# Kernel optimization log

Measured on AMD Instinct MI355X. Metric: run time of the kernel, lower is better.

The kernel has to match this reference:

```python
import jax, jax.numpy as jnp
import numpy as np

N_NODES = 100000
N_EDGES = 1600000
IN_CH, HID_CH, OUT_CH = 8, 64, 2


def setup_inputs() -> dict:
    key = jax.random.key(0)
    ks = jax.random.split(key, 8)
    x = jax.random.normal(ks[0], (N_NODES, IN_CH), dtype=jnp.float32)
    edge_index = jax.random.randint(ks[1], (2, N_EDGES), 0, N_NODES, dtype=jnp.int64)
    s1 = 1.0 / np.sqrt(IN_CH)
    s2 = 1.0 / np.sqrt(HID_CH)
    W_l1 = jax.random.normal(ks[2], (HID_CH, IN_CH), dtype=jnp.float32) * s1
    b_l1 = jax.random.normal(ks[3], (HID_CH,), dtype=jnp.float32) * s1
    W_r1 = jax.random.normal(ks[4], (HID_CH, IN_CH), dtype=jnp.float32) * s1
    W_l2 = jax.random.normal(ks[5], (OUT_CH, HID_CH), dtype=jnp.float32) * s2
    b_l2 = jax.random.normal(ks[6], (OUT_CH,), dtype=jnp.float32) * s2
    W_r2 = jax.random.normal(ks[7], (OUT_CH, HID_CH), dtype=jnp.float32) * s2
    return {"x": x, "edge_index": edge_index, "W_l1": W_l1, "b_l1": b_l1,
            "W_r1": W_r1, "W_l2": W_l2, "b_l2": b_l2, "W_r2": W_r2}


def _sage_conv(x, edge_index, W_l, b_l, W_r):
    # PyG SAGEConv (aggr='mean', root_weight=True):
    #   out = lin_l(mean_{j in N(i)} x_j) + lin_r(x_i)
    src, dst = edge_index[0], edge_index[1]
    n = x.shape[0]
    msgs = x[src]                                             # [E, F] gather
    summed = jax.ops.segment_sum(msgs, dst, num_segments=n)   # [N, F] scatter-add
    cnt = jax.ops.segment_sum(jnp.ones((src.shape[0],), x.dtype), dst,
                              num_segments=n)                 # [N]
    aggr = summed / jnp.maximum(cnt, 1.0)[:, None]            # scatter-mean
    return aggr @ W_l.T + b_l + x @ W_r.T


def reference(x, edge_index, W_l1, b_l1, W_r1, W_l2, b_l2, W_r2):
    h = _sage_conv(x, edge_index, W_l1, b_l1, W_r1)
    h = jax.nn.relu(h)
    # Dropout(0.3) is identity in eval mode (deterministic baseline).
    out = _sage_conv(h, edge_index, W_l2, b_l2, W_r2)
    return out
```

## Files before the change

kernel.cpp:

```cpp
#include <hip/hip_runtime.h>

#define N_NODES 100000
#define N_EDGES 1600000
#define IN_CH 8
#define HID_CH 64
#define OUT_CH 2

#define R2   512
#define RN   196
#define CAP  3584
#define BB   256
#define BCHUNK (N_EDGES / BB)

#define WS_CURSOR 0
#define WS_BUCKET 512
#define WS_OFFDEG (512 + R2 * CAP)
#define WS_G      (WS_OFFDEG + R2 * RN)

__global__ __launch_bounds__(512) void bucket_kernel(
        const int* __restrict__ src, const int* __restrict__ dst,
        int* __restrict__ cursor, int* __restrict__ bucket) {
    __shared__ int cnt[R2];
    __shared__ int base[R2];
    __shared__ int cur[R2];
    for (int i = threadIdx.x; i < R2; i += 512) { cnt[i] = 0; cur[i] = 0; }
    __syncthreads();
    const int* dch = dst + (size_t)blockIdx.x * BCHUNK;
    const int* sch = src + (size_t)blockIdx.x * BCHUNK;
    for (int j = threadIdx.x; j < BCHUNK; j += 512)
        atomicAdd(&cnt[(unsigned)dch[j] / RN], 1);
    __syncthreads();
    if (threadIdx.x < R2) {
        int c = cnt[threadIdx.x];
        base[threadIdx.x] = (c > 0) ? atomicAdd(&cursor[threadIdx.x], c) : 0;
    }
    __syncthreads();
    for (int j = threadIdx.x; j < BCHUNK; j += 512) {
        unsigned d = (unsigned)dch[j];
        unsigned r = d / RN;
        unsigned dl = d - r * RN;
        int slot = base[r] + atomicAdd(&cur[r], 1);
        if (slot < CAP)
            bucket[(size_t)r * CAP + slot] = (int)((dl << 17) | (unsigned)sch[j]);
    }
}

__global__ __launch_bounds__(256) void sage1_range(
        const int* __restrict__ bucket_g, const int* __restrict__ cursor,
        const float* __restrict__ x,
        const float* __restrict__ W_l1, const float* __restrict__ b_l1,
        const float* __restrict__ W_r1,
        const float* __restrict__ W_l2, const float* __restrict__ b_l2,
        const float* __restrict__ W_r2,
        int* __restrict__ bucket_w, int* __restrict__ offdeg,
        float* __restrict__ g, float* __restrict__ out_rt) {
    __shared__ int raw[CAP];
    __shared__ int seg[CAP];
    __shared__ int cnt[RN];
    __shared__ int cur[RN];
    __shared__ int sscan[256];
    __shared__ float sWl[HID_CH * IN_CH];
    __shared__ float sWr[HID_CH * IN_CH];
    __shared__ float sb[HID_CH];
    __shared__ float sWl2[OUT_CH * HID_CH];
    __shared__ float sWr2[OUT_CH * HID_CH];
    __shared__ float sb2[OUT_CH];

    int tid = threadIdx.x;
    for (int i = tid; i < HID_CH * IN_CH; i += 256) {
        sWl[i] = W_l1[i];
        sWr[i] = W_r1[i];
    }
    for (int i = tid; i < HID_CH; i += 256) sb[i] = b_l1[i];
    for (int i = tid; i < OUT_CH * HID_CH; i += 256) {
        sWl2[i] = W_l2[i];
        sWr2[i] = W_r2[i];
    }
    if (tid < OUT_CH) sb2[tid] = b_l2[tid];

    int r = blockIdx.x;
    int len = cursor[r];
    if (len > CAP) len = CAP;
    const int* bin = bucket_g + (size_t)r * CAP;
    for (int j = tid; j < len; j += 256) raw[j] = bin[j];
    if (tid < RN) cnt[tid] = 0;
    __syncthreads();

    for (int j = tid; j < len; j += 256) atomicAdd(&cnt[raw[j] >> 17], 1);
    __syncthreads();

    int v = (tid < RN) ? cnt[tid] : 0;
    sscan[tid] = v;
    __syncthreads();
    for (int d = 1; d < 256; d <<= 1) {
        int t2 = (tid >= d) ? sscan[tid - d] : 0;
        __syncthreads();
        if (tid >= d) sscan[tid] += t2;
        __syncthreads();
    }
    int myoff = sscan[tid] - v;
    if (tid < RN) cur[tid] = myoff;
    __syncthreads();

    for (int j = tid; j < len; j += 256) {
        int w = raw[j];
        int dl = w >> 17;
        int pos = atomicAdd(&cur[dl], 1);
        seg[pos] = w & 0x1FFFF;
    }
    __syncthreads();

    int* binw = bucket_w + (size_t)r * CAP;
    for (int j = tid; j < len; j += 256) binw[j] = seg[j];

    int node = r * RN + tid;
    if (tid < RN && node < N_NODES) {
        int mycnt = cnt[tid];
        offdeg[node] = myoff | (mycnt << 16);

        float acc[IN_CH];
        #pragma unroll
        for (int c = 0; c < IN_CH; c++) acc[c] = 0.0f;
        for (int j = 0; j < mycnt; j++) {
            int s = seg[myoff + j];
            const float4* xs = (const float4*)(x + (size_t)s * IN_CH);
            float4 a = xs[0];
            float4 b = xs[1];
            acc[0] += a.x; acc[1] += a.y; acc[2] += a.z; acc[3] += a.w;
            acc[4] += b.x; acc[5] += b.y; acc[6] += b.z; acc[7] += b.w;
        }
        float inv = 1.0f / fmaxf((float)mycnt, 1.0f);
        float ag[IN_CH], xa[IN_CH];
        #pragma unroll
        for (int c = 0; c < IN_CH; c++) ag[c] = acc[c] * inv;
        const float4* xp = (const float4*)(x + (size_t)node * IN_CH);
        float4 x0 = xp[0], x1 = xp[1];
        xa[0] = x0.x; xa[1] = x0.y; xa[2] = x0.z; xa[3] = x0.w;
        xa[4] = x1.x; xa[5] = x1.y; xa[6] = x1.z; xa[7] = x1.w;

        float g0 = 0.f, g1 = 0.f, r0 = 0.f, r1 = 0.f;
        #pragma unroll 8
        for (int kk = 0; kk < HID_CH; kk++) {
            float hk = sb[kk];
            #pragma unroll
            for (int c = 0; c < IN_CH; c++) {
                hk += sWl[kk * IN_CH + c] * ag[c];
                hk += sWr[kk * IN_CH + c] * xa[c];
            }
            hk = fmaxf(hk, 0.0f);
            g0 += sWl2[kk] * hk;
            g1 += sWl2[HID_CH + kk] * hk;
            r0 += sWr2[kk] * hk;
            r1 += sWr2[HID_CH + kk] * hk;
        }
        g[(size_t)node * 2 + 0] = g0;
        g[(size_t)node * 2 + 1] = g1;
        float2 rt;
        rt.x = r0 + sb2[0];
        rt.y = r1 + sb2[1];
        *(float2*)(out_rt + (size_t)node * 2) = rt;
    }
}

__global__ __launch_bounds__(256) void sage2_range(
        const int* __restrict__ bucket_g, const int* __restrict__ cursor,
        const int* __restrict__ offdeg, const float* __restrict__ g,
        float* __restrict__ out) {
    __shared__ int seg[CAP];
    int tid = threadIdx.x;
    int r = blockIdx.x;
    int len = cursor[r];
    if (len > CAP) len = CAP;
    const int* bin = bucket_g + (size_t)r * CAP;
    for (int j = tid; j < len; j += 256) seg[j] = bin[j];
    __syncthreads();

    int node = r * RN + tid;
    if (tid < RN && node < N_NODES) {
        int od = offdeg[node];
        int o = od & 0xFFFF;
        int dn = od >> 16;
        float a0 = 0.f, a1 = 0.f;
        for (int j = 0; j < dn; j++) {
            int s = seg[o + j];
            float2 gv = *(const float2*)(g + (size_t)s * 2);
            a0 += gv.x;
            a1 += gv.y;
        }
        float inv = 1.0f / fmaxf((float)dn, 1.0f);
        float2 rt = *(const float2*)(out + (size_t)node * 2);
        float2 ov;
        ov.x = a0 * inv + rt.x;
        ov.y = a1 * inv + rt.y;
        *(float2*)(out + (size_t)node * 2) = ov;
    }
}

extern "C" void kernel_launch(void* const* d_in, const int* in_sizes, int n_in,
                              void* d_out, int out_size, void* d_ws, size_t ws_size,
                              hipStream_t stream) {
    const float* x    = (const float*)d_in[0];
    const int*   ei   = (const int*)d_in[1];
    const float* W_l1 = (const float*)d_in[2];
    const float* b_l1 = (const float*)d_in[3];
    const float* W_r1 = (const float*)d_in[4];
    const float* W_l2 = (const float*)d_in[5];
    const float* b_l2 = (const float*)d_in[6];
    const float* W_r2 = (const float*)d_in[7];
    float* out = (float*)d_out;

    const int* src = ei;
    const int* dst = ei + N_EDGES;

    int*   cursor = (int*)d_ws + WS_CURSOR;
    int*   bucket = (int*)d_ws + WS_BUCKET;
    int*   offdeg = (int*)d_ws + WS_OFFDEG;
    float* g      = (float*)d_ws + WS_G;

    hipMemsetAsync(cursor, 0, R2 * sizeof(int), stream);

    bucket_kernel<<<BB, 512, 0, stream>>>(src, dst, cursor, bucket);
    sage1_range<<<R2, 256, 0, stream>>>(bucket, cursor, x,
                                        W_l1, b_l1, W_r1, W_l2, b_l2, W_r2,
                                        bucket, offdeg, g, out);
    sage2_range<<<R2, 256, 0, stream>>>(bucket, cursor, offdeg, g, out);
}
```

Baseline: 140.7 us.

## Replace per-range counting sort with linked lists split across two threads per node

Instead of counting, scanning and scattering edges into per-node segments in shared memory, each edge is pushed onto a per-node linked list with atomicExch. Even and odd edge indices go to two separate lists, so two threads walk each node's neighbours and combine their partial sums with a lane shuffle. Blocks grow to 512 threads. The next and head arrays are written to global memory so the second layer can reuse the lists. This removes the block-wide scan and its barriers, but the list walk is a dependent pointer chase through shared memory and sage2 now loads twice as much per-bucket data.

```diff
diff --git a/kernel.cpp b/kernel.cpp
--- a/kernel.cpp
+++ b/kernel.cpp
@@ -8,14 +8,15 @@
 
 #define R2   512
 #define RN   196
+#define NL   (2 * RN)
 #define CAP  3584
 #define BB   256
 #define BCHUNK (N_EDGES / BB)
 
-#define WS_CURSOR 0
 #define WS_BUCKET 512
-#define WS_OFFDEG (512 + R2 * CAP)
-#define WS_G      (WS_OFFDEG + R2 * RN)
+#define WS_NEXT   (WS_BUCKET + R2 * CAP)
+#define WS_HEAD   (WS_NEXT + R2 * CAP)
+#define WS_G      (WS_HEAD + R2 * NL)
 
 __global__ __launch_bounds__(512) void bucket_kernel(
         const int* __restrict__ src, const int* __restrict__ dst,
@@ -45,20 +46,18 @@
     }
 }
 
-__global__ __launch_bounds__(256) void sage1_range(
-        const int* __restrict__ bucket_g, const int* __restrict__ cursor,
+__global__ __launch_bounds__(512) void sage1_range(
+        const int* __restrict__ bucket, const int* __restrict__ cursor,
         const float* __restrict__ x,
         const float* __restrict__ W_l1, const float* __restrict__ b_l1,
         const float* __restrict__ W_r1,
         const float* __restrict__ W_l2, const float* __restrict__ b_l2,
         const float* __restrict__ W_r2,
-        int* __restrict__ bucket_w, int* __restrict__ offdeg,
+        int* __restrict__ nextg, int* __restrict__ headg,
         float* __restrict__ g, float* __restrict__ out_rt) {
     __shared__ int raw[CAP];
-    __shared__ int seg[CAP];
-    __shared__ int cnt[RN];
-    __shared__ int cur[RN];
-    __shared__ int sscan[256];
+    __shared__ int nxt[CAP];
+    __shared__ int head[NL];
     __shared__ float sWl[HID_CH * IN_CH];
     __shared__ float sWr[HID_CH * IN_CH];
     __shared__ float sb[HID_CH];
@@ -67,69 +66,63 @@
     __shared__ float sb2[OUT_CH];
 
     int tid = threadIdx.x;
-    for (int i = tid; i < HID_CH * IN_CH; i += 256) {
+    for (int i = tid; i < HID_CH * IN_CH; i += 512) {
         sWl[i] = W_l1[i];
         sWr[i] = W_r1[i];
     }
-    for (int i = tid; i < HID_CH; i += 256) sb[i] = b_l1[i];
-    for (int i = tid; i < OUT_CH * HID_CH; i += 256) {
+    for (int i = tid; i < HID_CH; i += 512) sb[i] = b_l1[i];
+    for (int i = tid; i < OUT_CH * HID_CH; i += 512) {
         sWl2[i] = W_l2[i];
         sWr2[i] = W_r2[i];
     }
     if (tid < OUT_CH) sb2[tid] = b_l2[tid];
+    if (tid < NL) head[tid] = -1;
 
     int r = blockIdx.x;
     int len = cursor[r];
     if (len > CAP) len = CAP;
-    const int* bin = bucket_g + (size_t)r * CAP;
-    for (int j = tid; j < len; j += 256) raw[j] = bin[j];
-    if (tid < RN) cnt[tid] = 0;
-    __syncthreads();
-
-    for (int j = tid; j < len; j += 256) atomicAdd(&cnt[raw[j] >> 17], 1);
-    __syncthreads();
-
-    int v = (tid < RN) ? cnt[tid] : 0;
-    sscan[tid] = v;
-    __syncthreads();
-    for (int d = 1; d < 256; d <<= 1) {
-        int t2 = (tid >= d) ? sscan[tid - d] : 0;
-        __syncthreads();
-        if (tid >= d) sscan[tid] += t2;
-        __syncthreads();
-    }
-    int myoff = sscan[tid] - v;
-    if (tid < RN) cur[tid] = myoff;
-    __syncthreads();
-
-    for (int j = tid; j < len; j += 256) {
-        int w = raw[j];
-        int dl = w >> 17;
-        int pos = atomicAdd(&cur[dl], 1);
-        seg[pos] = w & 0x1FFFF;
-    }
-    __syncthreads();
-
-    int* binw = bucket_w + (size_t)r * CAP;
-    for (int j = tid; j < len; j += 256) binw[j] = seg[j];
-
-    int node = r * RN + tid;
-    if (tid < RN && node < N_NODES) {
-        int mycnt = cnt[tid];
-        offdeg[node] = myoff | (mycnt << 16);
-
-        float acc[IN_CH];
-        #pragma unroll
-        for (int c = 0; c < IN_CH; c++) acc[c] = 0.0f;
-        for (int j = 0; j < mycnt; j++) {
-            int s = seg[myoff + j];
+    const int* bin = bucket + (size_t)r * CAP;
+    for (int j = tid; j < len; j += 512) raw[j] = bin[j];
+    __syncthreads();
+
+    for (int j = tid; j < len; j += 512) {
+        int dl = raw[j] >> 17;
+        int old = atomicExch(&head[(j & 1) * RN + dl], j);
+        nxt[j] = old;
+    }
+    __syncthreads();
+
+    int* nw = nextg + (size_t)r * CAP;
+    for (int j = tid; j < len; j += 512) nw[j] = nxt[j];
+    if (tid < NL) headg[(size_t)r * NL + tid] = head[tid];
+
+    float acc[IN_CH];
+    #pragma unroll
+    for (int c = 0; c < IN_CH; c++) acc[c] = 0.0f;
+    int cnt = 0;
+    if (tid < NL) {
+        int nl = tid >> 1;
+        int k = tid & 1;
+        int j = head[k * RN + nl];
+        while (j >= 0) {
+            int j2 = nxt[j];
+            int s = raw[j] & 0x1FFFF;
             const float4* xs = (const float4*)(x + (size_t)s * IN_CH);
             float4 a = xs[0];
             float4 b = xs[1];
             acc[0] += a.x; acc[1] += a.y; acc[2] += a.z; acc[3] += a.w;
             acc[4] += b.x; acc[5] += b.y; acc[6] += b.z; acc[7] += b.w;
+            cnt++;
+            j = j2;
         }
-        float inv = 1.0f / fmaxf((float)mycnt, 1.0f);
+    }
+    #pragma unroll
+    for (int c = 0; c < IN_CH; c++) acc[c] += __shfl_xor(acc[c], 1);
+    cnt += __shfl_xor(cnt, 1);
+
+    int node = r * RN + (tid >> 1);
+    if (tid < NL && (tid & 1) == 0 && node < N_NODES) {
+        float inv = 1.0f / fmaxf((float)cnt, 1.0f);
         float ag[IN_CH], xa[IN_CH];
         #pragma unroll
         for (int c = 0; c < IN_CH; c++) ag[c] = acc[c] * inv;
@@ -162,37 +155,54 @@
     }
 }
 
-__global__ __launch_bounds__(256) void sage2_range(
-        const int* __restrict__ bucket_g, const int* __restrict__ cursor,
-        const int* __restrict__ offdeg, const float* __restrict__ g,
-        float* __restrict__ out) {
-    __shared__ int seg[CAP];
+__global__ __launch_bounds__(512) void sage2_range(
+        const int* __restrict__ bucket, const int* __restrict__ cursor,
+        const int* __restrict__ nextg, const int* __restrict__ headg,
+        const float* __restrict__ g, float* __restrict__ out) {
+    __shared__ int raw[CAP];
+    __shared__ int nxt[CAP];
+    __shared__ int head[NL];
     int tid = threadIdx.x;
     int r = blockIdx.x;
     int len = cursor[r];
     if (len > CAP) len = CAP;
-    const int* bin = bucket_g + (size_t)r * CAP;
-    for (int j = tid; j < len; j += 256) seg[j] = bin[j];
-    __syncthreads();
-
-    int node = r * RN + tid;
-    if (tid < RN && node < N_NODES) {
-        int od = offdeg[node];
-        int o = od & 0xFFFF;
-        int dn = od >> 16;
-        float a0 = 0.f, a1 = 0.f;
-        for (int j = 0; j < dn; j++) {
-            int s = seg[o + j];
+    const int* bin = bucket + (size_t)r * CAP;
+    const int* nr  = nextg + (size_t)r * CAP;
+    for (int j = tid; j < len; j += 512) {
+        raw[j] = bin[j];
+        nxt[j] = nr[j];
+    }
+    if (tid < NL) head[tid] = headg[(size_t)r * NL + tid];
+    __syncthreads();
+
+    float a0 = 0.f, a1 = 0.f;
+    int cnt = 0;
+    if (tid < NL) {
+        int nl = tid >> 1;
+        int k = tid & 1;
+        int j = head[k * RN + nl];
+        while (j >= 0) {
+            int j2 = nxt[j];
+            int s = raw[j] & 0x1FFFF;
             float2 gv = *(const float2*)(g + (size_t)s * 2);
             a0 += gv.x;
             a1 += gv.y;
+            cnt++;
+            j = j2;
         }
-        float inv = 1.0f / fmaxf((float)dn, 1.0f);
+    }
+    a0 += __shfl_xor(a0, 1);
+    a1 += __shfl_xor(a1, 1);
+    cnt += __shfl_xor(cnt, 1);
+
+    int node = r * RN + (tid >> 1);
+    if (tid < NL && (tid & 1) == 0 && node < N_NODES) {
+        float inv = 1.0f / fmaxf((float)cnt, 1.0f);
         float2 rt = *(const float2*)(out + (size_t)node * 2);
-        float2 ov;
-        ov.x = a0 * inv + rt.x;
-        ov.y = a1 * inv + rt.y;
-        *(float2*)(out + (size_t)node * 2) = ov;
+        float2 o;
+        o.x = a0 * inv + rt.x;
+        o.y = a1 * inv + rt.y;
+        *(float2*)(out + (size_t)node * 2) = o;
     }
 }
 
@@ -212,16 +222,17 @@
     const int* src = ei;
     const int* dst = ei + N_EDGES;
 
-    int*   cursor = (int*)d_ws + WS_CURSOR;
+    int*   cursor = (int*)d_ws;
     int*   bucket = (int*)d_ws + WS_BUCKET;
-    int*   offdeg = (int*)d_ws + WS_OFFDEG;
+    int*   nextg  = (int*)d_ws + WS_NEXT;
+    int*   headg  = (int*)d_ws + WS_HEAD;
     float* g      = (float*)d_ws + WS_G;
 
     hipMemsetAsync(cursor, 0, R2 * sizeof(int), stream);
 
     bucket_kernel<<<BB, 512, 0, stream>>>(src, dst, cursor, bucket);
-    sage1_range<<<R2, 256, 0, stream>>>(bucket, cursor, x,
+    sage1_range<<<R2, 512, 0, stream>>>(bucket, cursor, x,
                                         W_l1, b_l1, W_r1, W_l2, b_l2, W_r2,
-                                        bucket, offdeg, g, out);
-    sage2_range<<<R2, 256, 0, stream>>>(bucket, cursor, offdeg, g, out);
-}
+                                        nextg, headg, g, out);
+    sage2_range<<<R2, 512, 0, stream>>>(bucket, cursor, nextg, headg, g, out);
+}
```

New measurement: 140.3 us. No clear change (-0.3%).

## Use four lanes per node, smaller buckets, and a flat CSR-gather second layer

Applied to the files above, without the earlier changes.

Halves the bucket range size, doubling the bucket count, so sage1 runs 1024 blocks of 512 threads. Each destination node now gets four lanes that split its edge gather and its hidden-layer matmul, with the partial sums combined by shuffle reductions. The prefix scan becomes a wavefront shuffle scan over 128 entries instead of a 256-wide shared-memory scan with barriers. Layer 2 becomes a flat grid of four lanes per node that reads the CSR straight from global memory, with no per-block staging of the bucket in shared memory. This targets the low occupancy and serial per-thread edge loops, at the cost of extra shuffles and a tighter CAP=1920, which overflows more easily with skewed degrees.

```diff
diff --git a/kernel.cpp b/kernel.cpp
--- a/kernel.cpp
+++ b/kernel.cpp
@@ -6,15 +6,14 @@
 #define HID_CH 64
 #define OUT_CH 2
 
-#define R2   512
-#define RN   196
-#define CAP  3584
+#define R2   1024
+#define RN   98
+#define CAP  1920
 #define BB   256
 #define BCHUNK (N_EDGES / BB)
 
-#define WS_CURSOR 0
-#define WS_BUCKET 512
-#define WS_OFFDEG (512 + R2 * CAP)
+#define WS_BUCKET 1024
+#define WS_OFFDEG (WS_BUCKET + R2 * CAP)
 #define WS_G      (WS_OFFDEG + R2 * RN)
 
 __global__ __launch_bounds__(512) void bucket_kernel(
@@ -30,9 +29,9 @@
     for (int j = threadIdx.x; j < BCHUNK; j += 512)
         atomicAdd(&cnt[(unsigned)dch[j] / RN], 1);
     __syncthreads();
-    if (threadIdx.x < R2) {
-        int c = cnt[threadIdx.x];
-        base[threadIdx.x] = (c > 0) ? atomicAdd(&cursor[threadIdx.x], c) : 0;
+    for (int i = threadIdx.x; i < R2; i += 512) {
+        int c = cnt[i];
+        base[i] = (c > 0) ? atomicAdd(&cursor[i], c) : 0;
     }
     __syncthreads();
     for (int j = threadIdx.x; j < BCHUNK; j += 512) {
@@ -45,20 +44,21 @@
     }
 }
 
-__global__ __launch_bounds__(256) void sage1_range(
-        const int* __restrict__ bucket_g, const int* __restrict__ cursor,
+__global__ __launch_bounds__(512) void sage1_range(
+        const int* __restrict__ bucket, const int* __restrict__ cursor,
         const float* __restrict__ x,
         const float* __restrict__ W_l1, const float* __restrict__ b_l1,
         const float* __restrict__ W_r1,
         const float* __restrict__ W_l2, const float* __restrict__ b_l2,
         const float* __restrict__ W_r2,
-        int* __restrict__ bucket_w, int* __restrict__ offdeg,
+        int* __restrict__ csr, int* __restrict__ offdeg,
         float* __restrict__ g, float* __restrict__ out_rt) {
     __shared__ int raw[CAP];
     __shared__ int seg[CAP];
-    __shared__ int cnt[RN];
-    __shared__ int cur[RN];
-    __shared__ int sscan[256];
+    __shared__ int scnt[128];
+    __shared__ int soff[128];
+    __shared__ int scur[128];
+    __shared__ int wtot[2];
     __shared__ float sWl[HID_CH * IN_CH];
     __shared__ float sWr[HID_CH * IN_CH];
     __shared__ float sb[HID_CH];
@@ -67,69 +67,83 @@
     __shared__ float sb2[OUT_CH];
 
     int tid = threadIdx.x;
-    for (int i = tid; i < HID_CH * IN_CH; i += 256) {
+    for (int i = tid; i < HID_CH * IN_CH; i += 512) {
         sWl[i] = W_l1[i];
         sWr[i] = W_r1[i];
     }
-    for (int i = tid; i < HID_CH; i += 256) sb[i] = b_l1[i];
-    for (int i = tid; i < OUT_CH * HID_CH; i += 256) {
+    for (int i = tid; i < HID_CH; i += 512) sb[i] = b_l1[i];
+    for (int i = tid; i < OUT_CH * HID_CH; i += 512) {
         sWl2[i] = W_l2[i];
         sWr2[i] = W_r2[i];
     }
     if (tid < OUT_CH) sb2[tid] = b_l2[tid];
+    if (tid < 128) scnt[tid] = 0;
 
     int r = blockIdx.x;
     int len = cursor[r];
     if (len > CAP) len = CAP;
-    const int* bin = bucket_g + (size_t)r * CAP;
-    for (int j = tid; j < len; j += 256) raw[j] = bin[j];
-    if (tid < RN) cnt[tid] = 0;
-    __syncthreads();
-
-    for (int j = tid; j < len; j += 256) atomicAdd(&cnt[raw[j] >> 17], 1);
-    __syncthreads();
-
-    int v = (tid < RN) ? cnt[tid] : 0;
-    sscan[tid] = v;
-    __syncthreads();
-    for (int d = 1; d < 256; d <<= 1) {
-        int t2 = (tid >= d) ? sscan[tid - d] : 0;
-        __syncthreads();
-        if (tid >= d) sscan[tid] += t2;
-        __syncthreads();
-    }
-    int myoff = sscan[tid] - v;
-    if (tid < RN) cur[tid] = myoff;
-    __syncthreads();
-
-    for (int j = tid; j < len; j += 256) {
+    const int* bin = bucket + (size_t)r * CAP;
+    for (int j = tid; j < len; j += 512) raw[j] = bin[j];
+    __syncthreads();
+
+    for (int j = tid; j < len; j += 512) atomicAdd(&scnt[raw[j] >> 17], 1);
+    __syncthreads();
+
+    int lane = tid & 63;
+    if (tid < 128) {
+        int v = scnt[tid];
+        int incl = v;
+        #pragma unroll
+        for (int d = 1; d < 64; d <<= 1) {
+            int t2 = __shfl_up(incl, d);
+            if (lane >= d) incl += t2;
+        }
+        if (lane == 63) wtot[tid >> 6] = incl;
+        soff[tid] = incl - v;
+    }
+    __syncthreads();
+    if (tid < 128) {
+        int o = soff[tid] + ((tid >= 64) ? wtot[0] : 0);
+        soff[tid] = o;
+        scur[tid] = o;
+    }
+    __syncthreads();
+
+    for (int j = tid; j < len; j += 512) {
         int w = raw[j];
-        int dl = w >> 17;
-        int pos = atomicAdd(&cur[dl], 1);
-        seg[pos] = w & 0x1FFFF;
-    }
-    __syncthreads();
-
-    int* binw = bucket_w + (size_t)r * CAP;
-    for (int j = tid; j < len; j += 256) binw[j] = seg[j];
-
-    int node = r * RN + tid;
-    if (tid < RN && node < N_NODES) {
-        int mycnt = cnt[tid];
-        offdeg[node] = myoff | (mycnt << 16);
+        int p = atomicAdd(&scur[w >> 17], 1);
+        seg[p] = w & 0x1FFFF;
+    }
+    __syncthreads();
+
+    int* cw = csr + (size_t)r * CAP;
+    for (int j = tid; j < len; j += 512) cw[j] = seg[j];
+
+    int q = tid >> 2;
+    int l = tid & 3;
+    int node = r * RN + q;
+    if (q < RN && node < N_NODES) {
+        int o = soff[q];
+        int dn = scnt[q];
+        if (l == 0) offdeg[node] = o | (dn << 16);
 
         float acc[IN_CH];
         #pragma unroll
         for (int c = 0; c < IN_CH; c++) acc[c] = 0.0f;
-        for (int j = 0; j < mycnt; j++) {
-            int s = seg[myoff + j];
+        for (int j = o + l; j < o + dn; j += 4) {
+            int s = seg[j];
             const float4* xs = (const float4*)(x + (size_t)s * IN_CH);
             float4 a = xs[0];
             float4 b = xs[1];
             acc[0] += a.x; acc[1] += a.y; acc[2] += a.z; acc[3] += a.w;
             acc[4] += b.x; acc[5] += b.y; acc[6] += b.z; acc[7] += b.w;
         }
-        float inv = 1.0f / fmaxf((float)mycnt, 1.0f);
+        #pragma unroll
+        for (int c = 0; c < IN_CH; c++) {
+            acc[c] += __shfl_xor(acc[c], 1);
+            acc[c] += __shfl_xor(acc[c], 2);
+        }
+        float inv = 1.0f / fmaxf((float)dn, 1.0f);
         float ag[IN_CH], xa[IN_CH];
         #pragma unroll
         for (int c = 0; c < IN_CH; c++) ag[c] = acc[c] * inv;
@@ -139,8 +153,9 @@
         xa[4] = x1.x; xa[5] = x1.y; xa[6] = x1.z; xa[7] = x1.w;
 
         float g0 = 0.f, g1 = 0.f, r0 = 0.f, r1 = 0.f;
-        #pragma unroll 8
-        for (int kk = 0; kk < HID_CH; kk++) {
+        int k0 = l * 16;
+        #pragma unroll 4
+        for (int kk = k0; kk < k0 + 16; kk++) {
             float hk = sb[kk];
             #pragma unroll
             for (int c = 0; c < IN_CH; c++) {
@@ -153,40 +168,43 @@
             r0 += sWr2[kk] * hk;
             r1 += sWr2[HID_CH + kk] * hk;
         }
-        g[(size_t)node * 2 + 0] = g0;
-        g[(size_t)node * 2 + 1] = g1;
-        float2 rt;
-        rt.x = r0 + sb2[0];
-        rt.y = r1 + sb2[1];
-        *(float2*)(out_rt + (size_t)node * 2) = rt;
-    }
-}
-
-__global__ __launch_bounds__(256) void sage2_range(
-        const int* __restrict__ bucket_g, const int* __restrict__ cursor,
-        const int* __restrict__ offdeg, const float* __restrict__ g,
-        float* __restrict__ out) {
-    __shared__ int seg[CAP];
-    int tid = threadIdx.x;
-    int r = blockIdx.x;
-    int len = cursor[r];
-    if (len > CAP) len = CAP;
-    const int* bin = bucket_g + (size_t)r * CAP;
-    for (int j = tid; j < len; j += 256) seg[j] = bin[j];
-    __syncthreads();
-
-    int node = r * RN + tid;
-    if (tid < RN && node < N_NODES) {
-        int od = offdeg[node];
-        int o = od & 0xFFFF;
-        int dn = od >> 16;
-        float a0 = 0.f, a1 = 0.f;
-        for (int j = 0; j < dn; j++) {
-            int s = seg[o + j];
-            float2 gv = *(const float2*)(g + (size_t)s * 2);
-            a0 += gv.x;
-            a1 += gv.y;
-        }
+        g0 += __shfl_xor(g0, 1); g0 += __shfl_xor(g0, 2);
+        g1 += __shfl_xor(g1, 1); g1 += __shfl_xor(g1, 2);
+        r0 += __shfl_xor(r0, 1); r0 += __shfl_xor(r0, 2);
+        r1 += __shfl_xor(r1, 1); r1 += __shfl_xor(r1, 2);
+        if (l == 0) {
+            g[(size_t)node * 2 + 0] = g0;
+            g[(size_t)node * 2 + 1] = g1;
+            float2 rt;
+            rt.x = r0 + sb2[0];
+            rt.y = r1 + sb2[1];
+            *(float2*)(out_rt + (size_t)node * 2) = rt;
+        }
+    }
+}
+
+__global__ __launch_bounds__(256) void sage2_kernel(
+        const int* __restrict__ csr, const int* __restrict__ offdeg,
+        const float* __restrict__ g, float* __restrict__ out) {
+    int t = blockIdx.x * blockDim.x + threadIdx.x;
+    int node = t >> 2;
+    int l = t & 3;
+    if (node >= N_NODES) return;
+    int r = node / RN;
+    int od = offdeg[node];
+    int o = od & 0xFFFF;
+    int dn = od >> 16;
+    const int* seg = csr + (size_t)r * CAP;
+    float a0 = 0.f, a1 = 0.f;
+    for (int j = o + l; j < o + dn; j += 4) {
+        int s = seg[j];
+        float2 gv = *(const float2*)(g + (size_t)s * 2);
+        a0 += gv.x;
+        a1 += gv.y;
+    }
+    a0 += __shfl_xor(a0, 1); a0 += __shfl_xor(a0, 2);
+    a1 += __shfl_xor(a1, 1); a1 += __shfl_xor(a1, 2);
+    if (l == 0) {
         float inv = 1.0f / fmaxf((float)dn, 1.0f);
         float2 rt = *(const float2*)(out + (size_t)node * 2);
         float2 ov;
@@ -212,7 +230,7 @@
     const int* src = ei;
     const int* dst = ei + N_EDGES;
 
-    int*   cursor = (int*)d_ws + WS_CURSOR;
+    int*   cursor = (int*)d_ws;
     int*   bucket = (int*)d_ws + WS_BUCKET;
     int*   offdeg = (int*)d_ws + WS_OFFDEG;
     float* g      = (float*)d_ws + WS_G;
@@ -220,8 +238,8 @@
     hipMemsetAsync(cursor, 0, R2 * sizeof(int), stream);
 
     bucket_kernel<<<BB, 512, 0, stream>>>(src, dst, cursor, bucket);
-    sage1_range<<<R2, 256, 0, stream>>>(bucket, cursor, x,
+    sage1_range<<<R2, 512, 0, stream>>>(bucket, cursor, x,
                                         W_l1, b_l1, W_r1, W_l2, b_l2, W_r2,
-                                        bucket, offdeg, g, out);
-    sage2_range<<<R2, 256, 0, stream>>>(bucket, cursor, offdeg, g, out);
-}
+                                        bucket , offdeg, g, out);
+    sage2_kernel<<<(4 * N_NODES + 255) / 256, 256, 0, stream>>>(bucket, offdeg, g, out);
+}
```

Result: faster. 136.7 us, median of 2 (-2.9%).
